# Kernel optimization log

Measured on AMD Instinct MI355X. Metric: run time of the kernel, lower is better.

Reference implementation:

```python
import jax, jax.numpy as jnp
import numpy as np

N_NODES = 50000
N_EDGES = 1600000
DIM = 512


def setup_inputs() -> dict:
    key = jax.random.key(0)
    k1, k2, k3, k4, k5 = jax.random.split(key, 5)
    x = jax.random.normal(k1, (N_NODES, DIM), dtype=jnp.float32)
    adj_rows = jax.random.randint(k2, (N_EDGES,), 0, N_NODES, dtype=jnp.int32)
    adj_cols = jax.random.randint(k3, (N_EDGES,), 0, N_NODES, dtype=jnp.int32)
    adj_vals = jax.random.uniform(k4, (N_EDGES,), dtype=jnp.float32)
    # fc1 weight [out_dim, in_dim], kaiming-normal-ish init
    weight = jax.random.normal(k5, (DIM, DIM), dtype=jnp.float32) * np.float32(np.sqrt(2.0 / DIM))
    scale = jnp.full((1,), 1.5, dtype=jnp.float32)
    return {"x": x, "adj_rows": adj_rows, "adj_cols": adj_cols,
            "adj_vals": adj_vals, "weight": weight, "scale": scale}


def reference(x, adj_rows, adj_cols, adj_vals, weight, scale):
    # dropout in eval mode -> identity
    N, D = x.shape
    # dense linear: y = x @ W^T
    y = jnp.einsum('nd,od->no', x, weight)
    # sparse adj @ y  (COO SpMM via gather + segment_sum)
    y = jax.ops.segment_sum(adj_vals[:, None] * y[adj_cols], adj_rows,
                            num_segments=N)
    # sp_norm: mean-center over nodes, scale by global RMS^{-1} * (1+scale) * sqrt(D)
    y_t = y - jnp.mean(y, axis=0, keepdims=True)
    y_norm = jnp.mean(jnp.sum(y_t * y_t, axis=1)) ** -0.5
    y = y_t * y_norm * (1.0 + scale) * jnp.float32(np.sqrt(D))
    # activation (relu), then residual (input_dim == output_dim)
    y = jax.nn.relu(y)
    return y + x
```

## Files before the change

kernel.cpp:

```cpp
#include <hip/hip_runtime.h>
#include <hip/hip_bf16.h>
#include <cstdint>
#include <cstddef>

#define N_NODES 50000
#define DIM 512
#define N_EDGES 1600000
#define NB N_NODES

typedef __bf16 bf16;
typedef __bf16 bf16x8 __attribute__((ext_vector_type(8)));
typedef __bf16 bf16x4 __attribute__((ext_vector_type(4)));
typedef float floatx4 __attribute__((ext_vector_type(4)));
typedef float floatx2 __attribute__((ext_vector_type(2)));
typedef unsigned int uintx2 __attribute__((ext_vector_type(2)));
typedef unsigned int uintx4 __attribute__((ext_vector_type(4)));

__global__ void cast_kernel(const float* __restrict__ in, bf16* __restrict__ out, int n4) {
    int i = blockIdx.x * blockDim.x + threadIdx.x;
    if (i >= n4) return;
    float4 v = reinterpret_cast<const float4*>(in)[i];
    bf16x4 o;
    o[0] = (bf16)v.x; o[1] = (bf16)v.y; o[2] = (bf16)v.z; o[3] = (bf16)v.w;
    reinterpret_cast<bf16x4*>(out)[i] = o;
}

__global__ void hist_kernel(const int* __restrict__ rows, int* __restrict__ cnt, int E) {
    int i = blockIdx.x * blockDim.x + threadIdx.x;
    if (i < E) atomicAdd(&cnt[rows[i]], 1);
}

__global__ __launch_bounds__(1024) void scanA_kernel(const int* __restrict__ cnt,
                                                     int* __restrict__ row_start,
                                                     int* __restrict__ blksum, int n) {
    __shared__ int s[1024];
    const int t = threadIdx.x;
    int i = blockIdx.x * 1024 + t;
    int v = (i < n) ? cnt[i] : 0;
    s[t] = v;
    __syncthreads();
    for (int off = 1; off < 1024; off <<= 1) {
        int u = (t >= off) ? s[t - off] : 0;
        __syncthreads();
        s[t] += u;
        __syncthreads();
    }
    if (i < n) row_start[i] = s[t] - v;
    if (t == 1023) blksum[blockIdx.x] = s[1023];
}

__global__ __launch_bounds__(1024) void scanB_kernel(const int* __restrict__ blksum,
                                                     int* __restrict__ blkoff, int nb) {
    __shared__ int s[1024];
    const int t = threadIdx.x;
    const int base = t * 2;
    int a = (base < nb) ? blksum[base] : 0;
    int b = (base + 1 < nb) ? blksum[base + 1] : 0;
    s[t] = a + b;
    __syncthreads();
    for (int off = 1; off < 1024; off <<= 1) {
        int u = (t >= off) ? s[t - off] : 0;
        __syncthreads();
        s[t] += u;
        __syncthreads();
    }
    int excl = (t == 0) ? 0 : s[t - 1];
    if (base < nb) blkoff[base] = excl;
    if (base + 1 < nb) blkoff[base + 1] = excl + a;
}

__global__ __launch_bounds__(1024) void scanC_kernel(int* __restrict__ row_start,
                                                     const int* __restrict__ blkoff,
                                                     int* __restrict__ cursor, int n) {
    int i = blockIdx.x * 1024 + threadIdx.x;
    if (i >= n) return;
    int v = row_start[i] + blkoff[i >> 10];
    row_start[i] = v;
    cursor[i] = v;
    if (i == n - 1) row_start[n] = N_EDGES;
}

__global__ void scatter_kernel(const int* __restrict__ rows, const int* __restrict__ cols,
                               const float* __restrict__ vals, int* __restrict__ cursor,
                               unsigned long long* __restrict__ ecv, int E) {
    int i = blockIdx.x * blockDim.x + threadIdx.x;
    if (i >= E) return;
    int r = rows[i];
    int p = atomicAdd(&cursor[r], 1);
    unsigned long long packed =
        (unsigned long long)(unsigned int)cols[i] |
        ((unsigned long long)(unsigned int)__float_as_uint(vals[i]) << 32);
    __builtin_nontemporal_store(packed, &ecv[p]);
}

__global__ __launch_bounds__(512) void gemm_kernel(const float* __restrict__ A,
                                                   const bf16* __restrict__ B,
                                                   bf16* __restrict__ C) {
    __shared__ bf16 lB[512 * 32];
    const int t = threadIdx.x;
    const int wave = t >> 6;
    const int lane = t & 63;
    const int rowBase = blockIdx.x * 128;
    const int wm = (wave >> 1) * 32;
    const int wn = (wave & 1) * 256;
    const int l15 = lane & 15;
    const int koct = (lane >> 4) * 8;

    floatx4 acc[2][16] = {};

    for (int k0 = 0; k0 < DIM; k0 += 32) {
#pragma unroll
        for (int j = 0; j < 4; j++) {
            int idx = j * 512 + t;
            int n = idx >> 2;
            int ko = (idx & 3) * 8;
            const bf16* g = B + (size_t)n * DIM + k0 + ko;
            bf16* l = lB + (size_t)j * 4096 + wave * 512;
            __builtin_amdgcn_global_load_lds(
                (const __attribute__((address_space(1))) void*)g,
                (__attribute__((address_space(3))) void*)l, 16, 0, 0);
        }
        bf16x8 af[2];
#pragma unroll
        for (int i = 0; i < 2; i++) {
            int row = rowBase + wm + i * 16 + l15;
            if (row > N_NODES - 1) row = N_NODES - 1;
            const float* ga = A + (size_t)row * DIM + k0 + koct;
            float4 fa = *reinterpret_cast<const float4*>(ga);
            float4 fb = *reinterpret_cast<const float4*>(ga + 4);
            bf16x8 v;
            v[0] = (bf16)fa.x; v[1] = (bf16)fa.y; v[2] = (bf16)fa.z; v[3] = (bf16)fa.w;
            v[4] = (bf16)fb.x; v[5] = (bf16)fb.y; v[6] = (bf16)fb.z; v[7] = (bf16)fb.w;
            af[i] = v;
        }
        __syncthreads();
#pragma unroll
        for (int nt = 0; nt < 16; nt++) {
            const bf16* bp = lB + (size_t)(wn + nt * 16 + l15) * 32 + koct;
            bf16x8 bf = *reinterpret_cast<const bf16x8*>(bp);
            acc[0][nt] = __builtin_amdgcn_mfma_f32_16x16x32_bf16(af[0], bf, acc[0][nt], 0, 0, 0);
            acc[1][nt] = __builtin_amdgcn_mfma_f32_16x16x32_bf16(af[1], bf, acc[1][nt], 0, 0, 0);
        }
        __syncthreads();
    }
    const int rquad = (lane >> 4) * 4;
#pragma unroll
    for (int i = 0; i < 2; i++) {
#pragma unroll
        for (int reg = 0; reg < 4; reg++) {
            int gr = rowBase + wm + i * 16 + rquad + reg;
            if (gr >= N_NODES) continue;
#pragma unroll
            for (int nt = 0; nt < 16; nt++) {
                int gc = wn + nt * 16 + l15;
                C[(size_t)gr * DIM + gc] = (bf16)acc[i][nt][reg];
            }
        }
    }
}

__device__ __forceinline__ float blo(uint32_t w) { return __uint_as_float(w << 16); }
__device__ __forceinline__ float bhi(uint32_t w) { return __uint_as_float(w & 0xffff0000u); }

__device__ __forceinline__ void fmac4(float* acc, unsigned long long e, const uintx2& w) {
    float v = __uint_as_float((uint32_t)(e >> 32));
    acc[0] += v * blo(w[0]); acc[1] += v * bhi(w[0]);
    acc[2] += v * blo(w[1]); acc[3] += v * bhi(w[1]);
}

__global__ __launch_bounds__(256) void spmm_kernel(const int* __restrict__ row_start,
                                                   const unsigned long long* __restrict__ ecv,
                                                   const bf16* __restrict__ y,
                                                   float* __restrict__ y2, int dimOff) {
    const int wave = threadIdx.x >> 6;
    const int lane = threadIdx.x & 63;
    const int r = blockIdx.x * 4 + wave;
    const int s = row_start[r];
    const int e = row_start[r + 1];
    float acc[4] = {0.f, 0.f, 0.f, 0.f};
    const uintx2* yb = reinterpret_cast<const uintx2*>(
        reinterpret_cast<const char*>(y) + (size_t)dimOff * 2 + (size_t)lane * 8);

    int i = s;
    for (; i + 7 < e; i += 8) {
        unsigned long long e0 = __builtin_nontemporal_load(&ecv[i]);
        unsigned long long e1 = __builtin_nontemporal_load(&ecv[i + 1]);
        unsigned long long e2 = __builtin_nontemporal_load(&ecv[i + 2]);
        unsigned long long e3 = __builtin_nontemporal_load(&ecv[i + 3]);
        unsigned long long e4 = __builtin_nontemporal_load(&ecv[i + 4]);
        unsigned long long e5 = __builtin_nontemporal_load(&ecv[i + 5]);
        unsigned long long e6 = __builtin_nontemporal_load(&ecv[i + 6]);
        unsigned long long e7 = __builtin_nontemporal_load(&ecv[i + 7]);
        uintx2 w0 = yb[(size_t)(uint32_t)e0 * 128];
        uintx2 w1 = yb[(size_t)(uint32_t)e1 * 128];
        uintx2 w2 = yb[(size_t)(uint32_t)e2 * 128];
        uintx2 w3 = yb[(size_t)(uint32_t)e3 * 128];
        uintx2 w4 = yb[(size_t)(uint32_t)e4 * 128];
        uintx2 w5 = yb[(size_t)(uint32_t)e5 * 128];
        uintx2 w6 = yb[(size_t)(uint32_t)e6 * 128];
        uintx2 w7 = yb[(size_t)(uint32_t)e7 * 128];
        fmac4(acc, e0, w0); fmac4(acc, e1, w1); fmac4(acc, e2, w2); fmac4(acc, e3, w3);
        fmac4(acc, e4, w4); fmac4(acc, e5, w5); fmac4(acc, e6, w6); fmac4(acc, e7, w7);
    }
    for (; i < e; i++) {
        unsigned long long e0 = __builtin_nontemporal_load(&ecv[i]);
        uintx2 w0 = yb[(size_t)(uint32_t)e0 * 128];
        fmac4(acc, e0, w0);
    }
    floatx4 o; o[0] = acc[0]; o[1] = acc[1]; o[2] = acc[2]; o[3] = acc[3];
    floatx4* out = reinterpret_cast<floatx4*>(y2 + (size_t)r * DIM + dimOff + lane * 4);
    __builtin_nontemporal_store(o, out);
}

__global__ __launch_bounds__(256) void reduce_kernel(const float* __restrict__ y2,
                                                     float* __restrict__ colsum,
                                                     float* __restrict__ totsq) {
    const int t = threadIdx.x;
    const int d2 = t * 2;
    float c0 = 0.f, c1 = 0.f, sq = 0.f;
    for (int r = blockIdx.x; r < N_NODES; r += gridDim.x) {
        floatx2 v = __builtin_nontemporal_load(
            reinterpret_cast<const floatx2*>(y2 + (size_t)r * DIM + d2));
        c0 += v[0]; c1 += v[1];
        sq += v[0] * v[0] + v[1] * v[1];
    }
    atomicAdd(&colsum[d2], c0);
    atomicAdd(&colsum[d2 + 1], c1);
    __shared__ float ssq[256];
    ssq[t] = sq;
    __syncthreads();
    for (int off = 128; off > 0; off >>= 1) {
        if (t < off) ssq[t] += ssq[t + off];
        __syncthreads();
    }
    if (t == 0) atomicAdd(totsq, ssq[0]);
}

__global__ void scalar_kernel(const float* __restrict__ colsum, const float* __restrict__ totsq,
                              const float* __restrict__ scale, float* __restrict__ sfac) {
    __shared__ float sm[512];
    const int t = threadIdx.x;
    float mu = colsum[t] * (1.0f / N_NODES);
    sm[t] = mu * mu;
    __syncthreads();
    for (int off = 256; off > 0; off >>= 1) {
        if (t < off) sm[t] += sm[t + off];
        __syncthreads();
    }
    if (t == 0) {
        float var = totsq[0] * (1.0f / N_NODES) - sm[0];
        sfac[0] = rsqrtf(var) * (1.0f + scale[0]) * sqrtf((float)DIM);
    }
}

__global__ void final_kernel(float* __restrict__ y2, const float* __restrict__ x,
                             const float* __restrict__ colsum, const float* __restrict__ sfac,
                             int n4) {
    int i = blockIdx.x * blockDim.x + threadIdx.x;
    if (i >= n4) return;
    const float invN = 1.0f / N_NODES;
    floatx4 v = __builtin_nontemporal_load(reinterpret_cast<floatx4*>(y2) + i);
    floatx4 xv = __builtin_nontemporal_load(reinterpret_cast<const floatx4*>(x) + i);
    float4 mu = reinterpret_cast<const float4*>(colsum)[i & 127];
    float s = sfac[0];
    v[0] = fmaxf((v[0] - mu.x * invN) * s, 0.0f) + xv[0];
    v[1] = fmaxf((v[1] - mu.y * invN) * s, 0.0f) + xv[1];
    v[2] = fmaxf((v[2] - mu.z * invN) * s, 0.0f) + xv[2];
    v[3] = fmaxf((v[3] - mu.w * invN) * s, 0.0f) + xv[3];
    __builtin_nontemporal_store(v, reinterpret_cast<floatx4*>(y2) + i);
}

extern "C" void kernel_launch(void* const* d_in, const int* in_sizes, int n_in,
                              void* d_out, int out_size, void* d_ws, size_t ws_size,
                              hipStream_t stream) {
    const float* x        = (const float*)d_in[0];
    const int*   adj_rows = (const int*)d_in[1];
    const int*   adj_cols = (const int*)d_in[2];
    const float* adj_vals = (const float*)d_in[3];
    const float* weight   = (const float*)d_in[4];
    const float* scale    = (const float*)d_in[5];
    float* out = (float*)d_out;

    char* ws = (char*)d_ws;
    size_t off = 0;
    auto alloc = [&](size_t b) {
        char* p = ws + off;
        off += (b + 255) & ~(size_t)255;
        return p;
    };
    const int nblk = (NB + 1023) / 1024;
    bf16*  y         = (bf16*)alloc((size_t)N_NODES * DIM * 2);
    unsigned long long* ecv = (unsigned long long*)alloc((size_t)N_EDGES * 8);
    bf16*  Wb        = (bf16*)alloc((size_t)DIM * DIM * 2);
    int*   cnt       = (int*)alloc((size_t)NB * 4);
    int*   cursor    = cnt;
    int*   row_start = (int*)alloc((size_t)(NB + 1) * 4);
    int*   blksum    = (int*)alloc((size_t)nblk * 4);
    int*   blkoff    = (int*)alloc((size_t)nblk * 4);
    float* stats     = (float*)alloc(514 * 4);
    float* colsum    = stats;
    float* totsq     = stats + 512;
    float* sfac      = stats + 513;
    (void)ws_size; (void)in_sizes; (void)n_in; (void)out_size;

    hipMemsetAsync(cnt, 0, (size_t)NB * 4, stream);
    hipMemsetAsync(stats, 0, 514 * 4, stream);

    const int n4x = N_NODES * DIM / 4;
    const int n4w = DIM * DIM / 4;
    cast_kernel<<<(n4w + 255) / 256, 256, 0, stream>>>(weight, Wb, n4w);

    hist_kernel<<<(N_EDGES + 255) / 256, 256, 0, stream>>>(adj_rows, cnt, N_EDGES);
    scanA_kernel<<<nblk, 1024, 0, stream>>>(cnt, row_start, blksum, NB);
    scanB_kernel<<<1, 1024, 0, stream>>>(blksum, blkoff, nblk);
    scanC_kernel<<<nblk, 1024, 0, stream>>>(row_start, blkoff, cursor, NB);
    scatter_kernel<<<(N_EDGES + 255) / 256, 256, 0, stream>>>(adj_rows, adj_cols, adj_vals,
                                                              cursor, ecv, N_EDGES);

    gemm_kernel<<<(N_NODES + 127) / 128, 512, 0, stream>>>(x, Wb, y);

    spmm_kernel<<<N_NODES / 4, 256, 0, stream>>>(row_start, ecv, y, out, 0);
    spmm_kernel<<<N_NODES / 4, 256, 0, stream>>>(row_start, ecv, y, out, 256);

    reduce_kernel<<<256, 256, 0, stream>>>(out, colsum, totsq);
    scalar_kernel<<<1, 512, 0, stream>>>(colsum, totsq, scale, sfac);
    final_kernel<<<(n4x + 255) / 256, 256, 0, stream>>>(out, x, colsum, sfac, n4x);
}
```

Before: 818.5 us.

## Merge SpMM column halves into one pass and retile GEMM to 64-row blocks

The two SpMM launches, each covering half of the columns, become one launch. Each lane now gathers 16 bytes (8 bf16) per neighbor, so the edge list is read once instead of twice and gathers are wider, but unroll depth drops from 8 to 4 edges. The GEMM block shrinks from 128 to 64 rows, with each wave covering 128 columns instead of 256. This halves the accumulator registers and doubles the block count, at the cost of reloading the weight tile into LDS once per 64 rows instead of per 128. Nontemporal hints are removed from the edge stores and loads, and the reduce grid is doubled.

```diff
diff --git a/kernel.cpp b/kernel.cpp
--- a/kernel.cpp
+++ b/kernel.cpp
@@ -13,8 +13,6 @@
 typedef __bf16 bf16x4 __attribute__((ext_vector_type(4)));
 typedef float floatx4 __attribute__((ext_vector_type(4)));
 typedef float floatx2 __attribute__((ext_vector_type(2)));
-typedef unsigned int uintx2 __attribute__((ext_vector_type(2)));
-typedef unsigned int uintx4 __attribute__((ext_vector_type(4)));
 
 __global__ void cast_kernel(const float* __restrict__ in, bf16* __restrict__ out, int n4) {
     int i = blockIdx.x * blockDim.x + threadIdx.x;
@@ -82,15 +80,12 @@
 
 __global__ void scatter_kernel(const int* __restrict__ rows, const int* __restrict__ cols,
                                const float* __restrict__ vals, int* __restrict__ cursor,
-                               unsigned long long* __restrict__ ecv, int E) {
+                               int2* __restrict__ ecv, int E) {
     int i = blockIdx.x * blockDim.x + threadIdx.x;
     if (i >= E) return;
     int r = rows[i];
     int p = atomicAdd(&cursor[r], 1);
-    unsigned long long packed =
-        (unsigned long long)(unsigned int)cols[i] |
-        ((unsigned long long)(unsigned int)__float_as_uint(vals[i]) << 32);
-    __builtin_nontemporal_store(packed, &ecv[p]);
+    ecv[p] = make_int2(cols[i], __float_as_int(vals[i]));
 }
 
 __global__ __launch_bounds__(512) void gemm_kernel(const float* __restrict__ A,
@@ -100,13 +95,13 @@
     const int t = threadIdx.x;
     const int wave = t >> 6;
     const int lane = t & 63;
-    const int rowBase = blockIdx.x * 128;
-    const int wm = (wave >> 1) * 32;
-    const int wn = (wave & 1) * 256;
+    const int rowBase = blockIdx.x * 64;
+    const int wmBase = (wave >> 2) * 32;
+    const int wn = (wave & 3) * 128;
     const int l15 = lane & 15;
     const int koct = (lane >> 4) * 8;
 
-    floatx4 acc[2][16] = {};
+    floatx4 acc[2][8] = {};
 
     for (int k0 = 0; k0 < DIM; k0 += 32) {
 #pragma unroll
@@ -123,7 +118,7 @@
         bf16x8 af[2];
 #pragma unroll
         for (int i = 0; i < 2; i++) {
-            int row = rowBase + wm + i * 16 + l15;
+            int row = rowBase + wmBase + i * 16 + l15;
             if (row > N_NODES - 1) row = N_NODES - 1;
             const float* ga = A + (size_t)row * DIM + k0 + koct;
             float4 fa = *reinterpret_cast<const float4*>(ga);
@@ -135,7 +130,7 @@
         }
         __syncthreads();
 #pragma unroll
-        for (int nt = 0; nt < 16; nt++) {
+        for (int nt = 0; nt < 8; nt++) {
             const bf16* bp = lB + (size_t)(wn + nt * 16 + l15) * 32 + koct;
             bf16x8 bf = *reinterpret_cast<const bf16x8*>(bp);
             acc[0][nt] = __builtin_amdgcn_mfma_f32_16x16x32_bf16(af[0], bf, acc[0][nt], 0, 0, 0);
@@ -148,10 +143,10 @@
     for (int i = 0; i < 2; i++) {
 #pragma unroll
         for (int reg = 0; reg < 4; reg++) {
-            int gr = rowBase + wm + i * 16 + rquad + reg;
+            int gr = rowBase + wmBase + i * 16 + rquad + reg;
             if (gr >= N_NODES) continue;
 #pragma unroll
-            for (int nt = 0; nt < 16; nt++) {
+            for (int nt = 0; nt < 8; nt++) {
                 int gc = wn + nt * 16 + l15;
                 C[(size_t)gr * DIM + gc] = (bf16)acc[i][nt][reg];
             }
@@ -162,54 +157,45 @@
 __device__ __forceinline__ float blo(uint32_t w) { return __uint_as_float(w << 16); }
 __device__ __forceinline__ float bhi(uint32_t w) { return __uint_as_float(w & 0xffff0000u); }
 
-__device__ __forceinline__ void fmac4(float* acc, unsigned long long e, const uintx2& w) {
-    float v = __uint_as_float((uint32_t)(e >> 32));
-    acc[0] += v * blo(w[0]); acc[1] += v * bhi(w[0]);
-    acc[2] += v * blo(w[1]); acc[3] += v * bhi(w[1]);
+__device__ __forceinline__ void fmac8(float* acc, float v, const uint4& w) {
+    acc[0] += v * blo(w.x); acc[1] += v * bhi(w.x);
+    acc[2] += v * blo(w.y); acc[3] += v * bhi(w.y);
+    acc[4] += v * blo(w.z); acc[5] += v * bhi(w.z);
+    acc[6] += v * blo(w.w); acc[7] += v * bhi(w.w);
 }
 
 __global__ __launch_bounds__(256) void spmm_kernel(const int* __restrict__ row_start,
-                                                   const unsigned long long* __restrict__ ecv,
+                                                   const int2* __restrict__ ecv,
                                                    const bf16* __restrict__ y,
-                                                   float* __restrict__ y2, int dimOff) {
+                                                   float* __restrict__ y2) {
     const int wave = threadIdx.x >> 6;
     const int lane = threadIdx.x & 63;
     const int r = blockIdx.x * 4 + wave;
     const int s = row_start[r];
     const int e = row_start[r + 1];
-    float acc[4] = {0.f, 0.f, 0.f, 0.f};
-    const uintx2* yb = reinterpret_cast<const uintx2*>(
-        reinterpret_cast<const char*>(y) + (size_t)dimOff * 2 + (size_t)lane * 8);
+    float acc[8] = {0.f, 0.f, 0.f, 0.f, 0.f, 0.f, 0.f, 0.f};
+    const uint32_t* yb = reinterpret_cast<const uint32_t*>(y);
 
     int i = s;
-    for (; i + 7 < e; i += 8) {
-        unsigned long long e0 = __builtin_nontemporal_load(&ecv[i]);
-        unsigned long long e1 = __builtin_nontemporal_load(&ecv[i + 1]);
-        unsigned long long e2 = __builtin_nontemporal_load(&ecv[i + 2]);
-        unsigned long long e3 = __builtin_nontemporal_load(&ecv[i + 3]);
-        unsigned long long e4 = __builtin_nontemporal_load(&ecv[i + 4]);
-        unsigned long long e5 = __builtin_nontemporal_load(&ecv[i + 5]);
-        unsigned long long e6 = __builtin_nontemporal_load(&ecv[i + 6]);
-        unsigned long long e7 = __builtin_nontemporal_load(&ecv[i + 7]);
-        uintx2 w0 = yb[(size_t)(uint32_t)e0 * 128];
-        uintx2 w1 = yb[(size_t)(uint32_t)e1 * 128];
-        uintx2 w2 = yb[(size_t)(uint32_t)e2 * 128];
-        uintx2 w3 = yb[(size_t)(uint32_t)e3 * 128];
-        uintx2 w4 = yb[(size_t)(uint32_t)e4 * 128];
-        uintx2 w5 = yb[(size_t)(uint32_t)e5 * 128];
-        uintx2 w6 = yb[(size_t)(uint32_t)e6 * 128];
-        uintx2 w7 = yb[(size_t)(uint32_t)e7 * 128];
-        fmac4(acc, e0, w0); fmac4(acc, e1, w1); fmac4(acc, e2, w2); fmac4(acc, e3, w3);
-        fmac4(acc, e4, w4); fmac4(acc, e5, w5); fmac4(acc, e6, w6); fmac4(acc, e7, w7);
+    for (; i + 3 < e; i += 4) {
+        int2 e0 = ecv[i], e1 = ecv[i + 1], e2 = ecv[i + 2], e3 = ecv[i + 3];
+        uint4 w0 = *reinterpret_cast<const uint4*>(yb + (size_t)e0.x * 256 + lane * 4);
+        uint4 w1 = *reinterpret_cast<const uint4*>(yb + (size_t)e1.x * 256 + lane * 4);
+        uint4 w2 = *reinterpret_cast<const uint4*>(yb + (size_t)e2.x * 256 + lane * 4);
+        uint4 w3 = *reinterpret_cast<const uint4*>(yb + (size_t)e3.x * 256 + lane * 4);
+        fmac8(acc, __int_as_float(e0.y), w0);
+        fmac8(acc, __int_as_float(e1.y), w1);
+        fmac8(acc, __int_as_float(e2.y), w2);
+        fmac8(acc, __int_as_float(e3.y), w3);
     }
     for (; i < e; i++) {
-        unsigned long long e0 = __builtin_nontemporal_load(&ecv[i]);
-        uintx2 w0 = yb[(size_t)(uint32_t)e0 * 128];
-        fmac4(acc, e0, w0);
-    }
-    floatx4 o; o[0] = acc[0]; o[1] = acc[1]; o[2] = acc[2]; o[3] = acc[3];
-    floatx4* out = reinterpret_cast<floatx4*>(y2 + (size_t)r * DIM + dimOff + lane * 4);
-    __builtin_nontemporal_store(o, out);
+        int2 e0 = ecv[i];
+        uint4 w0 = *reinterpret_cast<const uint4*>(yb + (size_t)e0.x * 256 + lane * 4);
+        fmac8(acc, __int_as_float(e0.y), w0);
+    }
+    float4* out = reinterpret_cast<float4*>(y2 + (size_t)r * DIM + lane * 8);
+    out[0] = make_float4(acc[0], acc[1], acc[2], acc[3]);
+    out[1] = make_float4(acc[4], acc[5], acc[6], acc[7]);
 }
 
 __global__ __launch_bounds__(256) void reduce_kernel(const float* __restrict__ y2,
@@ -290,7 +276,7 @@
     };
     const int nblk = (NB + 1023) / 1024;
     bf16*  y         = (bf16*)alloc((size_t)N_NODES * DIM * 2);
-    unsigned long long* ecv = (unsigned long long*)alloc((size_t)N_EDGES * 8);
+    int2*  ecv       = (int2*)alloc((size_t)N_EDGES * 8);
     bf16*  Wb        = (bf16*)alloc((size_t)DIM * DIM * 2);
     int*   cnt       = (int*)alloc((size_t)NB * 4);
     int*   cursor    = cnt;
@@ -317,12 +303,11 @@
     scatter_kernel<<<(N_EDGES + 255) / 256, 256, 0, stream>>>(adj_rows, adj_cols, adj_vals,
                                                               cursor, ecv, N_EDGES);
 
-    gemm_kernel<<<(N_NODES + 127) / 128, 512, 0, stream>>>(x, Wb, y);
-
-    spmm_kernel<<<N_NODES / 4, 256, 0, stream>>>(row_start, ecv, y, out, 0);
-    spmm_kernel<<<N_NODES / 4, 256, 0, stream>>>(row_start, ecv, y, out, 256);
-
-    reduce_kernel<<<256, 256, 0, stream>>>(out, colsum, totsq);
+    gemm_kernel<<<(N_NODES + 63) / 64, 512, 0, stream>>>(x, Wb, y);
+
+    spmm_kernel<<<N_NODES / 4, 256, 0, stream>>>(row_start, ecv, y, out);
+
+    reduce_kernel<<<512, 256, 0, stream>>>(out, colsum, totsq);
     scalar_kernel<<<1, 512, 0, stream>>>(colsum, totsq, scale, sfac);
     final_kernel<<<(n4x + 255) / 256, 256, 0, stream>>>(out, x, colsum, sfac, n4x);
 }
```

After: 785.7 us. -4.0%, faster.
